# Performance work log

Measured on AMD Instinct MI355X. Metric: run time of the kernel, lower is better.

The kernel has to match this reference:

```python
import jax, jax.numpy as jnp
import numpy as np

C_IN = 34   # C*V = 2*17 channels after reshape
C_MID = 16
C_OUT = 3
N_LAYERS = 3
BN_EPS = 1e-5
NEG_SLOPE = 0.01


def setup_inputs() -> dict:
    key = jax.random.key(0)
    ks = jax.random.split(key, 16)
    B, C, T, V = 512, 2, 2048, 17
    s = 1.0 / np.sqrt(C_IN)
    inp = {
        "x": jax.random.normal(ks[0], (B, C, T, V), dtype=jnp.float32),
        # stacked per-layer 1x1-conv (linear) weights for Q/K/V of 3 attention layers
        "wq": jax.random.normal(ks[1], (N_LAYERS, C_IN, C_IN), dtype=jnp.float32) * s,
        "bq": jax.random.normal(ks[2], (N_LAYERS, C_IN), dtype=jnp.float32) * 0.02,
        "wk": jax.random.normal(ks[3], (N_LAYERS, C_IN, C_IN), dtype=jnp.float32) * s,
        "bk": jax.random.normal(ks[4], (N_LAYERS, C_IN), dtype=jnp.float32) * 0.02,
        "wv": jax.random.normal(ks[5], (N_LAYERS, C_IN, C_IN), dtype=jnp.float32) * s,
        "bv": jax.random.normal(ks[6], (N_LAYERS, C_IN), dtype=jnp.float32) * 0.02,
        # head: conv1 -> BN -> LeakyReLU -> conv2
        "w1": jax.random.normal(ks[7], (C_MID, C_IN), dtype=jnp.float32) * s,
        "b1": jax.random.normal(ks[8], (C_MID,), dtype=jnp.float32) * 0.02,
        "gamma": jnp.ones((C_MID,), dtype=jnp.float32),
        "beta": jnp.zeros((C_MID,), dtype=jnp.float32),
        "mean": jax.random.normal(ks[9], (C_MID,), dtype=jnp.float32) * 0.1,
        "var": jax.random.uniform(ks[10], (C_MID,), dtype=jnp.float32, minval=0.5, maxval=1.5),
        "w2": jax.random.normal(ks[11], (C_OUT, C_MID), dtype=jnp.float32) * (1.0 / np.sqrt(C_MID)),
        "b2": jax.random.normal(ks[12], (C_OUT,), dtype=jnp.float32) * 0.02,
    }
    return inp


def _conv1x1(w, b, h):
    # 1x1 Conv1d == linear over channel dim: (O,C) x (B,C,T) -> (B,O,T)
    return jnp.einsum('oc,bct->bot', w, h) + b[:, None]


def reference(x, wq, bq, wk, bk, wv, bv, w1, b1, gamma, beta, mean, var, w2, b2):
    B, C, T, V = x.shape
    h = x.transpose(0, 1, 3, 2).reshape(B, C * V, T)  # (B, 34, T)
    scale = 1.0 / (T ** 0.5)  # K.size(-1) ** 0.5 in the original
    for i in range(N_LAYERS):
        Q = _conv1x1(wq[i], bq[i], h)
        K = _conv1x1(wk[i], bk[i], h)
        Vv = _conv1x1(wv[i], bv[i], h)
        scores = jnp.einsum('bct,bdt->bcd', Q, K) * scale  # (B, 34, 34) channel attention
        attn = jax.nn.softmax(scores, axis=-1)
        h = jnp.einsum('bcd,bdt->bct', attn, Vv)
    y = _conv1x1(w1, b1, h)                               # (B, 16, T)
    inv = gamma / jnp.sqrt(var + BN_EPS)                  # inference-mode BatchNorm1d
    y = (y - mean[:, None]) * inv[:, None] + beta[:, None]
    y = jnp.where(y > 0, y, NEG_SLOPE * y)                # LeakyReLU
    return _conv1x1(w2, b2, y)                            # (B, 3, T)
```

## Files before the change

kernel.cpp:

```cpp
#include <hip/hip_runtime.h>

#define CV   34
#define TTOT 2048
#define NB   512
#define XB   69632
#define XC   34816

#define GS_STRIDE 1192
#define RB_OFF    (512 * 1192)
#define RB_STRIDE 576

typedef __attribute__((ext_vector_type(8))) short v8s;
typedef __attribute__((ext_vector_type(4))) float v4f;

__device__ __forceinline__ unsigned short f2bf(float f) {
    unsigned int u = __float_as_uint(f);
    u = u + 0x7FFFu + ((u >> 16) & 1u);
    return (unsigned short)(u >> 16);
}
__device__ __forceinline__ float bf2f(unsigned short s) {
    return __uint_as_float(((unsigned int)s) << 16);
}

__device__ __forceinline__ unsigned int cvtpk_bf16(float a, float b) {
    unsigned int r;
    asm("v_cvt_pk_bf16_f32 %0, %1, %2" : "=v"(r) : "v"(a), "v"(b));
    return r;
}

__device__ __forceinline__ void split8(const float (&f)[8], v8s* hi, v8s* lo) {
    union { unsigned int u[4]; v8s s; } H, L;
#pragma unroll
    for (int p = 0; p < 4; ++p) {
        float a = f[2 * p], b = f[2 * p + 1];
        unsigned int h = cvtpk_bf16(a, b);
        float ra = a - __uint_as_float(h << 16);
        float rb = b - __uint_as_float(h & 0xFFFF0000u);
        L.u[p] = cvtpk_bf16(ra, rb);
        H.u[p] = h;
    }
    *hi = H.s;
    *lo = L.s;
}

__device__ __forceinline__ void stage_chunk(const float* __restrict__ xb, int t0,
                                            float* rawbuf, int w, int lane) {
#pragma unroll
    for (int i = 0; i < 5; ++i) {
        int idx = i * 4 + w;
        if (idx < 17) {
            int fl = idx * 256 + lane * 4;
            int co = (fl >= 2176) ? 1 : 0;
            const float* g = xb + t0 * 17 + fl + co * 32640;
            __builtin_amdgcn_global_load_lds(
                (const __attribute__((address_space(1))) void*)g,
                (__attribute__((address_space(3))) void*)(rawbuf + idx * 256),
                16, 0, 0);
        }
    }
}

struct SmemGramB {
    float Gpart[4][34][36];
    float spart[4][36];
};

__global__ __launch_bounds__(256, 4) void k_gram(const float* __restrict__ x,
                                                 float* __restrict__ ws) {
    __shared__ __align__(16) union {
        float raw[2][4352];
        SmemGramB b;
    } sm;

    const int b    = blockIdx.x >> 2;
    const int seg  = blockIdx.x & 3;
    const int tid  = threadIdx.x;
    const int l    = tid & 63;
    const int w    = tid >> 6;
    const int row16 = l & 15;
    const int quad  = l >> 4;
    const float* xb = x + (size_t)b * XB;
    const int t0 = seg * 512;

    int offc[3];
#pragma unroll
    for (int r = 0; r < 3; ++r) {
        int c = r * 16 + row16;
        if (c > 33) c = 33;
        offc[r] = (c >= 17) ? (2159 + c) : c;
    }
    const int koff = w * 32 + quad * 8;

    v4f accG[3][3];
    v4f accS[3];
    v4f vz = {0.f, 0.f, 0.f, 0.f};
#pragma unroll
    for (int r = 0; r < 3; ++r) {
        accS[r] = vz;
#pragma unroll
        for (int c = 0; c < 3; ++c) accG[r][c] = vz;
    }
    v8s ones;
#pragma unroll
    for (int i = 0; i < 8; ++i) ones[i] = (short)0x3F80;

    stage_chunk(xb, t0, sm.raw[0], w, l);
    __syncthreads();

    for (int ch = 0; ch < 4; ++ch) {
        const int cur = ch & 1;
        if (ch < 3) stage_chunk(xb, t0 + (ch + 1) * 128, sm.raw[cur ^ 1], w, l);

        const float* rb = sm.raw[cur] + koff * 17;
        v8s fh[3], fl4[3];
#pragma unroll
        for (int r = 0; r < 3; ++r) {
            const float* p = rb + offc[r];
            float f[8];
#pragma unroll
            for (int e = 0; e < 8; ++e) f[e] = p[e * 17];
            split8(f, &fh[r], &fl4[r]);
        }
#pragma unroll
        for (int r = 0; r < 3; ++r) {
#pragma unroll
            for (int c = 0; c < 3; ++c) {
                accG[r][c] = __builtin_amdgcn_mfma_f32_16x16x32_bf16(fh[r],  fh[c],  accG[r][c], 0, 0, 0);
                accG[r][c] = __builtin_amdgcn_mfma_f32_16x16x32_bf16(fh[r],  fl4[c], accG[r][c], 0, 0, 0);
                accG[r][c] = __builtin_amdgcn_mfma_f32_16x16x32_bf16(fl4[r], fh[c],  accG[r][c], 0, 0, 0);
            }
            accS[r] = __builtin_amdgcn_mfma_f32_16x16x32_bf16(fh[r],  ones, accS[r], 0, 0, 0);
            accS[r] = __builtin_amdgcn_mfma_f32_16x16x32_bf16(fl4[r], ones, accS[r], 0, 0, 0);
        }
        __syncthreads();
    }

#pragma unroll
    for (int r = 0; r < 3; ++r) {
#pragma unroll
        for (int c = 0; c < 3; ++c) {
#pragma unroll
            for (int i = 0; i < 4; ++i) {
                int m = r * 16 + quad * 4 + i;
                int n = c * 16 + row16;
                if (m < 34 && n < 34) sm.b.Gpart[w][m][n] = accG[r][c][i];
            }
        }
        if (row16 == 0) {
#pragma unroll
            for (int i = 0; i < 4; ++i) {
                int m = r * 16 + quad * 4 + i;
                if (m < 34) sm.b.spart[w][m] = accS[r][i];
            }
        }
    }
    __syncthreads();
    float* gout = ws + (size_t)b * GS_STRIDE;
    for (int idx = tid; idx < 1156; idx += 256) {
        int m = idx / 34, n = idx - m * 34;
        atomicAdd(&gout[idx], sm.b.Gpart[0][m][n] + sm.b.Gpart[1][m][n] +
                              sm.b.Gpart[2][m][n] + sm.b.Gpart[3][m][n]);
    }
    if (tid < 34)
        atomicAdd(&gout[1156 + tid], sm.b.spart[0][tid] + sm.b.spart[1][tid] +
                                     sm.b.spart[2][tid] + sm.b.spart[3][tid]);
}


__device__ __forceinline__ void wave_mm(const float (*__restrict__ L)[36],
                                        const float (*__restrict__ R)[36],
                                        float (*__restrict__ D)[36], int l) {
    const int lr = l >> 4, lc = l & 15;
    const int i0 = lr * 9;
    const bool has3 = (lc < 3);
    const int j3 = has3 ? (lc + 32) : 0;
    float a0[9], a1[9], a2[9];
#pragma unroll
    for (int a = 0; a < 9; ++a) { a0[a] = 0.f; a1[a] = 0.f; a2[a] = 0.f; }
#pragma unroll
    for (int e0 = 0; e0 < 36; e0 += 4) {
        const float4 r0 = *(const float4*)&R[lc][e0];
        const float4 r1 = *(const float4*)&R[lc + 16][e0];
        const float4 r2 = *(const float4*)&R[j3][e0];
#pragma unroll
        for (int a = 0; a < 9; ++a) {
            const float4 lv = *(const float4*)&L[i0 + a][e0];
            a0[a] += lv.x * r0.x + lv.y * r0.y + lv.z * r0.z + lv.w * r0.w;
            a1[a] += lv.x * r1.x + lv.y * r1.y + lv.z * r1.z + lv.w * r1.w;
            a2[a] += lv.x * r2.x + lv.y * r2.y + lv.z * r2.z + lv.w * r2.w;
        }
    }
#pragma unroll
    for (int a = 0; a < 9; ++a) {
        D[i0 + a][lc]      = a0[a];
        D[i0 + a][lc + 16] = a1[a];
        if (has3) D[i0 + a][lc + 32] = a2[a];
    }
}

__device__ __forceinline__ void wave_mmG(const float* __restrict__ Wg, int nrows,
                                         const float (*__restrict__ R)[36],
                                         float (*__restrict__ D)[36],
                                         int transpose, int l) {
    const int lr = l >> 4, lc = l & 15;
    const int i0 = lr * 9;
    const bool has3 = (lc < 3);
    const int j3 = has3 ? (lc + 32) : 0;
    float a0[9], a1[9], a2[9];
#pragma unroll
    for (int a = 0; a < 9; ++a) { a0[a] = 0.f; a1[a] = 0.f; a2[a] = 0.f; }
#pragma unroll
    for (int e0 = 0; e0 < 32; e0 += 4) {
        const float4 r0 = *(const float4*)&R[lc][e0];
        const float4 r1 = *(const float4*)&R[lc + 16][e0];
        const float4 r2 = *(const float4*)&R[j3][e0];
#pragma unroll
        for (int a = 0; a < 9; ++a) {
            const int i = i0 + a;
            float2 la = make_float2(0.f, 0.f), lb = make_float2(0.f, 0.f);
            if (i < nrows) {
                la = *(const float2*)(Wg + i * 34 + e0);
                lb = *(const float2*)(Wg + i * 34 + e0 + 2);
            }
            a0[a] += la.x * r0.x + la.y * r0.y + lb.x * r0.z + lb.y * r0.w;
            a1[a] += la.x * r1.x + la.y * r1.y + lb.x * r1.z + lb.y * r1.w;
            a2[a] += la.x * r2.x + la.y * r2.y + lb.x * r2.z + lb.y * r2.w;
        }
    }
    {
        const float r00 = R[lc][32],      r01 = R[lc][33];
        const float r10 = R[lc + 16][32], r11 = R[lc + 16][33];
        const float r20 = R[j3][32],      r21 = R[j3][33];
#pragma unroll
        for (int a = 0; a < 9; ++a) {
            const int i = i0 + a;
            float2 la = make_float2(0.f, 0.f);
            if (i < nrows) la = *(const float2*)(Wg + i * 34 + 32);
            a0[a] += la.x * r00 + la.y * r01;
            a1[a] += la.x * r10 + la.y * r11;
            a2[a] += la.x * r20 + la.y * r21;
        }
    }
#pragma unroll
    for (int a = 0; a < 9; ++a) {
        const int i = i0 + a;
        if (transpose) {
            D[lc][i]      = a0[a];
            D[lc + 16][i] = a1[a];
            if (has3) D[lc + 32][i] = a2[a];
        } else {
            D[i][lc]      = a0[a];
            D[i][lc + 16] = a1[a];
            if (has3) D[i][lc + 32] = a2[a];
        }
    }
}

__global__ __launch_bounds__(64) void k_chain(
    const float* __restrict__ wq, const float* __restrict__ bq,
    const float* __restrict__ wk, const float* __restrict__ bk,
    const float* __restrict__ wv, const float* __restrict__ bv,
    const float* __restrict__ w1, const float* __restrict__ b1,
    const float* __restrict__ gamma, const float* __restrict__ beta,
    const float* __restrict__ mean, const float* __restrict__ var,
    float* __restrict__ ws) {
    __shared__ float SM[7][36][36];
    float (*G0b)[36] = SM[0];
    float (*At )[36] = SM[1];
    float (*Aq )[36] = SM[2];
    float (*Ak )[36] = SM[3];
    float (*AvT)[36] = SM[4];
    float (*S1 )[36] = SM[5];
    float (*Sc )[36] = SM[6];

    const int l = threadIdx.x;
    const int b = blockIdx.x;
    const float* gsb = ws + (size_t)b * GS_STRIDE;

    {
        const float4 z = make_float4(0.f, 0.f, 0.f, 0.f);
        float* base = &SM[0][0][0];
        for (int i = l * 4; i < 9072; i += 256) *(float4*)(base + i) = z;
    }
    __syncthreads();
    for (int idx = l; idx < 1156; idx += 64) {
        int m = idx / 34, n = idx - m * 34;
        G0b[m][n] = gsb[idx];
        Aq[m][n] = wq[idx];
        Ak[m][n] = wk[idx];
        AvT[n][m] = wv[idx];
    }
    if (l < 34) {
        float s = gsb[1156 + l];
        G0b[34][l] = s;
        G0b[l][34] = s;
        Aq[l][34]  = bq[l];
        Ak[l][34]  = bk[l];
        AvT[34][l] = bv[l];
    }
    if (l == 0) G0b[34][34] = 2048.0f;
    __syncthreads();

    for (int lyr = 0; lyr < 3; ++lyr) {
        if (lyr > 0) {
            const float* wql = wq + lyr * 1156;
            const float* wkl = wk + lyr * 1156;
            const float* wvl = wv + lyr * 1156;
            wave_mmG(wql, 34, At, Aq, 0, l);
            wave_mmG(wkl, 34, At, Ak, 0, l);
            wave_mmG(wvl, 34, At, AvT, 1, l);
            __syncthreads();
            if (l < 34) {
                Aq[l][34]  += bq[lyr * 34 + l];
                Ak[l][34]  += bk[lyr * 34 + l];
                AvT[34][l] += bv[lyr * 34 + l];
            }
            __syncthreads();
        }
        wave_mm(Aq, G0b, S1, l);
        __syncthreads();
        wave_mm(S1, Ak, Sc, l);
        __syncthreads();
        if (l < 34) {
            float f[36];
#pragma unroll
            for (int e0 = 0; e0 < 36; e0 += 4)
                *(float4*)&f[e0] = *(const float4*)&Sc[l][e0];
            const float scale = 0.022097086912079608f;
            float mx = -1e30f;
#pragma unroll
            for (int d = 0; d < 34; ++d) { f[d] *= scale; mx = fmaxf(mx, f[d]); }
            float sum = 0.f;
#pragma unroll
            for (int d = 0; d < 34; ++d) { float e = __expf(f[d] - mx); f[d] = e; sum += e; }
            float rs = 1.0f / sum;
#pragma unroll
            for (int d = 0; d < 34; ++d) f[d] *= rs;
            f[34] = 0.f; f[35] = 0.f;
#pragma unroll
            for (int e0 = 0; e0 < 36; e0 += 4)
                *(float4*)&Sc[l][e0] = *(const float4*)&f[e0];
        }
        __syncthreads();
        wave_mm(AvT, Sc, At, l);
        __syncthreads();
    }

    wave_mmG(w1, 16, At, S1, 0, l);
    __syncthreads();
    float* wb = ws + RB_OFF + (size_t)b * RB_STRIDE;
    if (l < 16) {
        float iv = gamma[l] * rsqrtf(var[l] + 1e-5f);
        float cyraw = S1[l][34] + b1[l];
        wb[512 + l] = (cyraw - mean[l]) * iv + beta[l];
        wb[528 + l] = S1[l][32] * iv;
        wb[544 + l] = S1[l][33] * iv;
    }
    unsigned short* wp = (unsigned short*)wb;
    for (int i = l; i < 512; i += 64) {
        int o = i >> 5, c = i & 31;
        float iv = gamma[o] * rsqrtf(var[o] + 1e-5f);
        float vv = S1[o][c] * iv;
        unsigned short hb = f2bf(vv);
        wp[i] = hb;
        wp[512 + i] = f2bf(vv - bf2f(hb));
    }
}

__global__ __launch_bounds__(256, 4) void k_out(const float* __restrict__ x,
                                                const float* __restrict__ w2,
                                                const float* __restrict__ b2,
                                                const float* __restrict__ ws,
                                                float* __restrict__ out) {
    __shared__ __align__(16) float raw[2][4352];

    const int tid  = threadIdx.x;
    const int b    = blockIdx.x >> 3;
    const int seg  = (blockIdx.x & 7) * 256;
    const int l    = tid & 63;
    const int w    = tid >> 6;
    const int quad = l >> 4;
    const int col  = l & 15;

    const float* wb = ws + RB_OFF + (size_t)b * RB_STRIDE;
    const unsigned short* wp = (const unsigned short*)wb;
    v8s aH = *(const v8s*)&wp[col * 32 + quad * 8];
    v8s aL = *(const v8s*)&wp[512 + col * 32 + quad * 8];
    float cyr[4], w2r[3][4], wy32r[4], wy33r[4];
#pragma unroll
    for (int i = 0; i < 4; ++i) {
        int o = quad * 4 + i;
        cyr[i]   = wb[512 + o];
        wy32r[i] = wb[528 + o];
        wy33r[i] = wb[544 + o];
#pragma unroll
        for (int p = 0; p < 3; ++p) w2r[p][i] = w2[p * 16 + o];
    }
    float b2r[3] = {b2[0], b2[1], b2[2]};
    const float* xb = x + (size_t)b * XB;

    int offq[8];
#pragma unroll
    for (int e = 0; e < 8; ++e) {
        int c = quad * 8 + e;
        offq[e] = (c >= 17) ? (2159 + c) : c;
    }

    stage_chunk(xb, seg, raw[0], w, l);
    __syncthreads();

    for (int ch = 0; ch < 2; ++ch) {
        if (ch == 0) stage_chunk(xb, seg + 128, raw[1], w, l);
        for (int tt = w; tt < 8; tt += 4) {
            const int tl = tt * 16 + col;
            const float* rbt = raw[ch] + tl * 17;
            float f[8];
#pragma unroll
            for (int e = 0; e < 8; ++e) f[e] = rbt[offq[e]];
            v8s bH, bL;
            split8(f, &bH, &bL);
            v4f acc = {0.f, 0.f, 0.f, 0.f};
            acc = __builtin_amdgcn_mfma_f32_16x16x32_bf16(aH, bH, acc, 0, 0, 0);
            acc = __builtin_amdgcn_mfma_f32_16x16x32_bf16(aH, bL, acc, 0, 0, 0);
            acc = __builtin_amdgcn_mfma_f32_16x16x32_bf16(aL, bH, acc, 0, 0, 0);
            float h32 = rbt[2191];
            float h33 = rbt[2192];
            float op[3] = {0, 0, 0};
#pragma unroll
            for (int i = 0; i < 4; ++i) {
                float y = acc[i] + cyr[i] + wy32r[i] * h32 + wy33r[i] * h33;
                float z = (y > 0.f) ? y : 0.01f * y;
#pragma unroll
                for (int p = 0; p < 3; ++p) op[p] += w2r[p][i] * z;
            }
#pragma unroll
            for (int p = 0; p < 3; ++p) {
                op[p] += __shfl_xor(op[p], 16);
                op[p] += __shfl_xor(op[p], 32);
            }
            if (l < 16) {
                int tg = seg + ch * 128 + tt * 16 + l;
#pragma unroll
                for (int p = 0; p < 3; ++p)
                    out[((size_t)b * 3 + p) * 2048 + tg] = op[p] + b2r[p];
            }
        }
        __syncthreads();
    }
}

extern "C" void kernel_launch(void* const* d_in, const int* in_sizes, int n_in,
                              void* d_out, int out_size, void* d_ws, size_t ws_size,
                              hipStream_t stream) {
    const float* x     = (const float*)d_in[0];
    const float* wq    = (const float*)d_in[1];
    const float* bq    = (const float*)d_in[2];
    const float* wk    = (const float*)d_in[3];
    const float* bk    = (const float*)d_in[4];
    const float* wv    = (const float*)d_in[5];
    const float* bv    = (const float*)d_in[6];
    const float* w1    = (const float*)d_in[7];
    const float* b1    = (const float*)d_in[8];
    const float* gamma = (const float*)d_in[9];
    const float* beta  = (const float*)d_in[10];
    const float* mean  = (const float*)d_in[11];
    const float* var   = (const float*)d_in[12];
    const float* w2    = (const float*)d_in[13];
    const float* b2    = (const float*)d_in[14];
    float* ws  = (float*)d_ws;
    float* out = (float*)d_out;

    hipMemsetAsync(d_ws, 0, (size_t)NB * GS_STRIDE * sizeof(float), stream);
    k_gram<<<dim3(2048), dim3(256), 0, stream>>>(x, ws);
    k_chain<<<dim3(512), dim3(64), 0, stream>>>(wq, bq, wk, bk, wv, bv,
                                                w1, b1, gamma, beta, mean, var, ws);
    k_out<<<dim3(4096), dim3(256), 0, stream>>>(x, w2, b2, ws, out);
}
```

Measured before the change: 345.0 us.

## Replace scalar FP32 small-matrix products in chain kernel with split-bf16 MFMA

The per-batch 36x36 matrix products in k_chain were computed with scalar FP32 FMAs by a single wave. They now use 16x16x32 bf16 MFMA instructions, with each operand split into a high and a low bf16 part so that three products approximate FP32 precision. The shared-memory layout moves to a padded stride of 44, and the global weights are staged into shared memory first. This trades extra conversion work, more shared memory and a small precision change for a shorter chain kernel, which is only part of the total time.

After: 316.6 us. 1.09x faster.

```diff
diff --git a/kernel.cpp b/kernel.cpp
--- a/kernel.cpp
+++ b/kernel.cpp
@@ -166,92 +166,87 @@
                                      sm.b.spart[2][tid] + sm.b.spart[3][tid]);
 }
 
-
-__device__ __forceinline__ void wave_mm(const float (*__restrict__ L)[36],
-                                        const float (*__restrict__ R)[36],
-                                        float (*__restrict__ D)[36], int l) {
-    const int lr = l >> 4, lc = l & 15;
-    const int i0 = lr * 9;
-    const bool has3 = (lc < 3);
-    const int j3 = has3 ? (lc + 32) : 0;
-    float a0[9], a1[9], a2[9];
-#pragma unroll
-    for (int a = 0; a < 9; ++a) { a0[a] = 0.f; a1[a] = 0.f; a2[a] = 0.f; }
-#pragma unroll
-    for (int e0 = 0; e0 < 36; e0 += 4) {
-        const float4 r0 = *(const float4*)&R[lc][e0];
-        const float4 r1 = *(const float4*)&R[lc + 16][e0];
-        const float4 r2 = *(const float4*)&R[j3][e0];
-#pragma unroll
-        for (int a = 0; a < 9; ++a) {
-            const float4 lv = *(const float4*)&L[i0 + a][e0];
-            a0[a] += lv.x * r0.x + lv.y * r0.y + lv.z * r0.z + lv.w * r0.w;
-            a1[a] += lv.x * r1.x + lv.y * r1.y + lv.z * r1.z + lv.w * r1.w;
-            a2[a] += lv.x * r2.x + lv.y * r2.y + lv.z * r2.z + lv.w * r2.w;
-        }
-    }
-#pragma unroll
-    for (int a = 0; a < 9; ++a) {
-        D[i0 + a][lc]      = a0[a];
-        D[i0 + a][lc + 16] = a1[a];
-        if (has3) D[i0 + a][lc + 32] = a2[a];
-    }
-}
-
-__device__ __forceinline__ void wave_mmG(const float* __restrict__ Wg, int nrows,
-                                         const float (*__restrict__ R)[36],
-                                         float (*__restrict__ D)[36],
-                                         int transpose, int l) {
-    const int lr = l >> 4, lc = l & 15;
-    const int i0 = lr * 9;
-    const bool has3 = (lc < 3);
-    const int j3 = has3 ? (lc + 32) : 0;
-    float a0[9], a1[9], a2[9];
-#pragma unroll
-    for (int a = 0; a < 9; ++a) { a0[a] = 0.f; a1[a] = 0.f; a2[a] = 0.f; }
-#pragma unroll
-    for (int e0 = 0; e0 < 32; e0 += 4) {
-        const float4 r0 = *(const float4*)&R[lc][e0];
-        const float4 r1 = *(const float4*)&R[lc + 16][e0];
-        const float4 r2 = *(const float4*)&R[j3][e0];
-#pragma unroll
-        for (int a = 0; a < 9; ++a) {
-            const int i = i0 + a;
-            float2 la = make_float2(0.f, 0.f), lb = make_float2(0.f, 0.f);
-            if (i < nrows) {
-                la = *(const float2*)(Wg + i * 34 + e0);
-                lb = *(const float2*)(Wg + i * 34 + e0 + 2);
-            }
-            a0[a] += la.x * r0.x + la.y * r0.y + lb.x * r0.z + lb.y * r0.w;
-            a1[a] += la.x * r1.x + la.y * r1.y + lb.x * r1.z + lb.y * r1.w;
-            a2[a] += la.x * r2.x + la.y * r2.y + lb.x * r2.z + lb.y * r2.w;
-        }
-    }
-    {
-        const float r00 = R[lc][32],      r01 = R[lc][33];
-        const float r10 = R[lc + 16][32], r11 = R[lc + 16][33];
-        const float r20 = R[j3][32],      r21 = R[j3][33];
-#pragma unroll
-        for (int a = 0; a < 9; ++a) {
-            const int i = i0 + a;
-            float2 la = make_float2(0.f, 0.f);
-            if (i < nrows) la = *(const float2*)(Wg + i * 34 + 32);
-            a0[a] += la.x * r00 + la.y * r01;
-            a1[a] += la.x * r10 + la.y * r11;
-            a2[a] += la.x * r20 + la.y * r21;
-        }
-    }
-#pragma unroll
-    for (int a = 0; a < 9; ++a) {
-        const int i = i0 + a;
-        if (transpose) {
-            D[lc][i]      = a0[a];
-            D[lc + 16][i] = a1[a];
-            if (has3) D[lc + 32][i] = a2[a];
-        } else {
-            D[i][lc]      = a0[a];
-            D[i][lc + 16] = a1[a];
-            if (has3) D[i][lc + 32] = a2[a];
+#define RST 44
+#define RSZ (36 * RST)
+#define R_G0 0
+#define R_At (1 * RSZ)
+#define R_Aq (2 * RSZ)
+#define R_Ak (3 * RSZ)
+#define R_Av (4 * RSZ)
+#define R_S1 (5 * RSZ)
+#define R_Sc (6 * RSZ)
+#define R_Wx (7 * RSZ)
+#define SMF  (8 * RSZ)
+
+__device__ __forceinline__ void ldfrag8(const float* p, v8s* hi, v8s* lo) {
+    float f[8];
+    *(float4*)&f[0] = *(const float4*)p;
+    *(float4*)&f[4] = *(const float4*)(p + 4);
+    split8(f, hi, lo);
+}
+
+__device__ __forceinline__ void ldfrag4(const float* p, int quad, v8s* hi, v8s* lo) {
+    union { unsigned int u[4]; v8s s; } H, L;
+#pragma unroll
+    for (int i = 0; i < 4; ++i) { H.u[i] = 0; L.u[i] = 0; }
+    if (quad == 0) {
+        float4 f = *(const float4*)p;
+        unsigned int h0 = cvtpk_bf16(f.x, f.y);
+        unsigned int h1 = cvtpk_bf16(f.z, f.w);
+        float r0 = f.x - __uint_as_float(h0 << 16);
+        float r1 = f.y - __uint_as_float(h0 & 0xFFFF0000u);
+        float r2 = f.z - __uint_as_float(h1 << 16);
+        float r3 = f.w - __uint_as_float(h1 & 0xFFFF0000u);
+        H.u[0] = h0; H.u[1] = h1;
+        L.u[0] = cvtpk_bf16(r0, r1);
+        L.u[1] = cvtpk_bf16(r2, r3);
+    }
+    *hi = H.s;
+    *lo = L.s;
+}
+
+__device__ __forceinline__ void mfma_mm(float* __restrict__ SMD, int Lo, int Ro,
+                                        int Do, int l, bool transD) {
+    const int lc = l & 15, quad = l >> 4;
+    v8s Bh0[3], Bl0[3], Bh1[3], Bl1[3];
+#pragma unroll
+    for (int tn = 0; tn < 3; ++tn) {
+        int r = tn * 16 + lc; r = r < 36 ? r : 35;
+        const float* p = SMD + Ro + r * RST;
+        ldfrag8(p + quad * 8, &Bh0[tn], &Bl0[tn]);
+        ldfrag4(p + 32, quad, &Bh1[tn], &Bl1[tn]);
+    }
+#pragma unroll
+    for (int tm = 0; tm < 3; ++tm) {
+        int r = tm * 16 + lc; r = r < 36 ? r : 35;
+        const float* p = SMD + Lo + r * RST;
+        v8s Ah0, Al0, Ah1, Al1;
+        ldfrag8(p + quad * 8, &Ah0, &Al0);
+        ldfrag4(p + 32, quad, &Ah1, &Al1);
+#pragma unroll
+        for (int tn = 0; tn < 3; ++tn) {
+            v4f acc = {0.f, 0.f, 0.f, 0.f};
+            acc = __builtin_amdgcn_mfma_f32_16x16x32_bf16(Ah0, Bh0[tn], acc, 0, 0, 0);
+            acc = __builtin_amdgcn_mfma_f32_16x16x32_bf16(Ah0, Bl0[tn], acc, 0, 0, 0);
+            acc = __builtin_amdgcn_mfma_f32_16x16x32_bf16(Al0, Bh0[tn], acc, 0, 0, 0);
+            acc = __builtin_amdgcn_mfma_f32_16x16x32_bf16(Ah1, Bh1[tn], acc, 0, 0, 0);
+            acc = __builtin_amdgcn_mfma_f32_16x16x32_bf16(Ah1, Bl1[tn], acc, 0, 0, 0);
+            acc = __builtin_amdgcn_mfma_f32_16x16x32_bf16(Al1, Bh1[tn], acc, 0, 0, 0);
+            if (!transD) {
+                int gcol = tn * 16 + lc;
+                if (gcol < 36) {
+#pragma unroll
+                    for (int i = 0; i < 4; ++i) {
+                        int grow = tm * 16 + quad * 4 + i;
+                        if (grow < 36) SMD[Do + grow * RST + gcol] = acc[i];
+                    }
+                }
+            } else {
+                int trow = tn * 16 + lc;
+                int tcol = tm * 16 + quad * 4;
+                if (trow < 36 && tcol < 36)
+                    *(v4f*)&SMD[Do + trow * RST + tcol] = acc;
+            }
         }
     }
 }
@@ -264,41 +259,32 @@
     const float* __restrict__ gamma, const float* __restrict__ beta,
     const float* __restrict__ mean, const float* __restrict__ var,
     float* __restrict__ ws) {
-    __shared__ float SM[7][36][36];
-    float (*G0b)[36] = SM[0];
-    float (*At )[36] = SM[1];
-    float (*Aq )[36] = SM[2];
-    float (*Ak )[36] = SM[3];
-    float (*AvT)[36] = SM[4];
-    float (*S1 )[36] = SM[5];
-    float (*Sc )[36] = SM[6];
-
+    __shared__ __align__(16) float SMD[SMF];
     const int l = threadIdx.x;
     const int b = blockIdx.x;
     const float* gsb = ws + (size_t)b * GS_STRIDE;
 
     {
         const float4 z = make_float4(0.f, 0.f, 0.f, 0.f);
-        float* base = &SM[0][0][0];
-        for (int i = l * 4; i < 9072; i += 256) *(float4*)(base + i) = z;
+        for (int i = l * 4; i < SMF; i += 256) *(float4*)(SMD + i) = z;
     }
     __syncthreads();
     for (int idx = l; idx < 1156; idx += 64) {
         int m = idx / 34, n = idx - m * 34;
-        G0b[m][n] = gsb[idx];
-        Aq[m][n] = wq[idx];
-        Ak[m][n] = wk[idx];
-        AvT[n][m] = wv[idx];
+        SMD[R_G0 + m * RST + n] = gsb[idx];
+        SMD[R_Aq + m * RST + n] = wq[idx];
+        SMD[R_Ak + m * RST + n] = wk[idx];
+        SMD[R_Av + n * RST + m] = wv[idx];
     }
     if (l < 34) {
         float s = gsb[1156 + l];
-        G0b[34][l] = s;
-        G0b[l][34] = s;
-        Aq[l][34]  = bq[l];
-        Ak[l][34]  = bk[l];
-        AvT[34][l] = bv[l];
-    }
-    if (l == 0) G0b[34][34] = 2048.0f;
+        SMD[R_G0 + 34 * RST + l] = s;
+        SMD[R_G0 + l * RST + 34] = s;
+        SMD[R_Aq + l * RST + 34] = bq[l];
+        SMD[R_Ak + l * RST + 34] = bk[l];
+        SMD[R_Av + 34 * RST + l] = bv[l];
+    }
+    if (l == 0) SMD[R_G0 + 34 * RST + 34] = 2048.0f;
     __syncthreads();
 
     for (int lyr = 0; lyr < 3; ++lyr) {
@@ -306,26 +292,33 @@
             const float* wql = wq + lyr * 1156;
             const float* wkl = wk + lyr * 1156;
             const float* wvl = wv + lyr * 1156;
-            wave_mmG(wql, 34, At, Aq, 0, l);
-            wave_mmG(wkl, 34, At, Ak, 0, l);
-            wave_mmG(wvl, 34, At, AvT, 1, l);
+            for (int idx = l; idx < 1156; idx += 64) {
+                int m = idx / 34, n = idx - m * 34;
+                SMD[R_S1 + m * RST + n] = wql[idx];
+                SMD[R_Sc + m * RST + n] = wkl[idx];
+                SMD[R_Wx + m * RST + n] = wvl[idx];
+            }
+            __syncthreads();
+            mfma_mm(SMD, R_S1, R_At, R_Aq, l, false);
+            mfma_mm(SMD, R_Sc, R_At, R_Ak, l, false);
+            mfma_mm(SMD, R_Wx, R_At, R_Av, l, true);
             __syncthreads();
             if (l < 34) {
-                Aq[l][34]  += bq[lyr * 34 + l];
-                Ak[l][34]  += bk[lyr * 34 + l];
-                AvT[34][l] += bv[lyr * 34 + l];
+                SMD[R_Aq + l * RST + 34] += bq[lyr * 34 + l];
+                SMD[R_Ak + l * RST + 34] += bk[lyr * 34 + l];
+                SMD[R_Av + 34 * RST + l] += bv[lyr * 34 + l];
             }
             __syncthreads();
         }
-        wave_mm(Aq, G0b, S1, l);
-        __syncthreads();
-        wave_mm(S1, Ak, Sc, l);
+        mfma_mm(SMD, R_Aq, R_G0, R_S1, l, false);
+        __syncthreads();
+        mfma_mm(SMD, R_S1, R_Ak, R_Sc, l, false);
         __syncthreads();
         if (l < 34) {
             float f[36];
 #pragma unroll
             for (int e0 = 0; e0 < 36; e0 += 4)
-                *(float4*)&f[e0] = *(const float4*)&Sc[l][e0];
+                *(float4*)&f[e0] = *(const float4*)&SMD[R_Sc + l * RST + e0];
             const float scale = 0.022097086912079608f;
             float mx = -1e30f;
 #pragma unroll
@@ -339,28 +332,37 @@
             f[34] = 0.f; f[35] = 0.f;
 #pragma unroll
             for (int e0 = 0; e0 < 36; e0 += 4)
-                *(float4*)&Sc[l][e0] = *(const float4*)&f[e0];
-        }
-        __syncthreads();
-        wave_mm(AvT, Sc, At, l);
-        __syncthreads();
-    }
-
-    wave_mmG(w1, 16, At, S1, 0, l);
+                *(float4*)&SMD[R_Sc + l * RST + e0] = *(const float4*)&f[e0];
+        } else if (l >= 36 && l < 54) {
+            int u = l - 36;
+            int row = 34 + u / 9, c4 = (u - (u / 9) * 9) * 4;
+            *(float4*)&SMD[R_Sc + row * RST + c4] = make_float4(0.f, 0.f, 0.f, 0.f);
+        }
+        __syncthreads();
+        mfma_mm(SMD, R_Av, R_Sc, R_At, l, false);
+        __syncthreads();
+    }
+
+    for (int idx = l; idx < 544; idx += 64) {
+        int m = idx / 34, n = idx - m * 34;
+        SMD[R_Sc + m * RST + n] = w1[idx];
+    }
+    __syncthreads();
+    mfma_mm(SMD, R_Sc, R_At, R_S1, l, false);
     __syncthreads();
     float* wb = ws + RB_OFF + (size_t)b * RB_STRIDE;
     if (l < 16) {
         float iv = gamma[l] * rsqrtf(var[l] + 1e-5f);
-        float cyraw = S1[l][34] + b1[l];
+        float cyraw = SMD[R_S1 + l * RST + 34] + b1[l];
         wb[512 + l] = (cyraw - mean[l]) * iv + beta[l];
-        wb[528 + l] = S1[l][32] * iv;
-        wb[544 + l] = S1[l][33] * iv;
+        wb[528 + l] = SMD[R_S1 + l * RST + 32] * iv;
+        wb[544 + l] = SMD[R_S1 + l * RST + 33] * iv;
     }
     unsigned short* wp = (unsigned short*)wb;
     for (int i = l; i < 512; i += 64) {
         int o = i >> 5, c = i & 31;
         float iv = gamma[o] * rsqrtf(var[o] + 1e-5f);
-        float vv = S1[o][c] * iv;
+        float vv = SMD[R_S1 + o * RST + c] * iv;
         unsigned short hb = f2bf(vv);
         wp[i] = hb;
         wp[512 + i] = f2bf(vv - bf2f(hb));
```
